# Optimization experiments

Measured on AMD Instinct MI355X. Metric: run time of the kernel, lower is better.

The kernel has to match this reference:

```python
import jax, jax.numpy as jnp
import numpy as np

N_NODES = 100000
N_EDGES = 3200000
D_IN = 256
D_OUT = 256


def setup_inputs() -> dict:
    key = jax.random.key(0)
    k1, k2, k3, k4, k5 = jax.random.split(key, 5)
    x = jax.random.normal(k1, (N_NODES, D_IN), dtype=jnp.float32)
    edge_row = jax.random.randint(k2, (N_EDGES,), 0, N_NODES, dtype=jnp.int32)
    edge_col = jax.random.randint(k3, (N_EDGES,), 0, N_NODES, dtype=jnp.int32)
    # normalized adjacency-like values in (0,1), scaled so rows sum ~1 on average
    edge_val = jax.random.uniform(k4, (N_EDGES,), dtype=jnp.float32) / 32.0
    # kaiming-uniform-like init: bound = sqrt(6 / ((1 + 5) * fan_in)) = 1/sqrt(fan_in)
    bound = 1.0 / np.sqrt(D_IN)
    weight = jax.random.uniform(k5, (D_IN, D_OUT), minval=-bound, maxval=bound, dtype=jnp.float32)
    return {"x": x, "edge_row": edge_row, "edge_col": edge_col,
            "edge_val": edge_val, "weight": weight}


def reference(x, edge_row, edge_col, edge_val, weight):
    # support = P @ X  (sparse COO spmm via gather + segment_sum)
    gathered = edge_val[:, None] * x[edge_col]          # [E, D_IN]
    support = jax.ops.segment_sum(gathered, edge_row, num_segments=N_NODES)  # [N, D_IN]
    # output = relu(support @ W)
    out = jax.nn.relu(support @ weight)                 # [N, D_OUT]
    return out
```

## Files before the change

### kernel.cpp

```cpp
#include <hip/hip_runtime.h>

#define N_NODES 100000
#define N_EDGES 3200000
#define D 256
#define NPAD 100032
#define BCAP 128

#define GEMM_BLKS (NPAD / 64)
#define NCHUNK 782
#define SCAT_BLKS (NCHUNK * 8)
#define ROWS_PER_G 12500

typedef __attribute__((ext_vector_type(8))) short short8;
typedef __attribute__((ext_vector_type(8))) unsigned short ushort8;
typedef __attribute__((ext_vector_type(4))) float f32x4;
typedef __attribute__((ext_vector_type(4))) int i32x4;

static __device__ __forceinline__ unsigned short f2bf(float f) {
  unsigned u = __float_as_uint(f);
  u += 0x7FFF + ((u >> 16) & 1);
  return (unsigned short)(u >> 16);
}
static __device__ __forceinline__ float bf2f(unsigned short h) {
  return __uint_as_float(((unsigned)h) << 16);
}

__global__ __launch_bounds__(64) void convert_wt(
    const float* __restrict__ W, ushort* __restrict__ wt) {
  int n = blockIdx.x;
  int k0 = threadIdx.x * 4;
  ushort4 o;
  o.x = f2bf(W[(size_t)(k0 + 0) * D + n]);
  o.y = f2bf(W[(size_t)(k0 + 1) * D + n]);
  o.z = f2bf(W[(size_t)(k0 + 2) * D + n]);
  o.w = f2bf(W[(size_t)(k0 + 3) * D + n]);
  *(ushort4*)(wt + (size_t)n * D + k0) = o;
}

__global__ __launch_bounds__(256) void gemm_scatter(
    const float* __restrict__ x, const ushort* __restrict__ wt,
    ushort* __restrict__ Y, const int* __restrict__ erow,
    const int* __restrict__ ecol, const float* __restrict__ eval_,
    int* __restrict__ cnt, unsigned* __restrict__ buckets) {
  __shared__ ushort sA[64][264];
  const int tid = threadIdx.x;

  if (blockIdx.x >= GEMM_BLKS) {
    const int sid = blockIdx.x - GEMM_BLKS;
    const int g = blockIdx.x & 7;
    const int chunk = sid >> 3;
    const int lo = g * ROWS_PER_G;
    const int hi = lo + ROWS_PER_G;
    const size_t ebase = (size_t)chunk * 4096;

    #pragma unroll
    for (int q = 0; q < 4; ++q) {
      size_t e0 = ebase + q * 1024 + tid * 4;
      if (e0 >= N_EDGES) continue;
      i32x4 r4 = *(const i32x4*)(erow + e0);
      bool m0 = (r4.x >= lo) & (r4.x < hi);
      bool m1 = (r4.y >= lo) & (r4.y < hi);
      bool m2 = (r4.z >= lo) & (r4.z < hi);
      bool m3 = (r4.w >= lo) & (r4.w < hi);
      if (!(m0 | m1 | m2 | m3)) continue;
      i32x4 c4 = *(const i32x4*)(ecol + e0);
      f32x4 v4 = *(const f32x4*)(eval_ + e0);
      if (m0) {
        int j = atomicAdd(&cnt[r4.x], 1);
        if (j < BCAP)
          buckets[(size_t)r4.x * BCAP + j] =
              ((unsigned)f2bf(v4.x) << 17) | (unsigned)c4.x;
      }
      if (m1) {
        int j = atomicAdd(&cnt[r4.y], 1);
        if (j < BCAP)
          buckets[(size_t)r4.y * BCAP + j] =
              ((unsigned)f2bf(v4.y) << 17) | (unsigned)c4.y;
      }
      if (m2) {
        int j = atomicAdd(&cnt[r4.z], 1);
        if (j < BCAP)
          buckets[(size_t)r4.z * BCAP + j] =
              ((unsigned)f2bf(v4.z) << 17) | (unsigned)c4.z;
      }
      if (m3) {
        int j = atomicAdd(&cnt[r4.w], 1);
        if (j < BCAP)
          buckets[(size_t)r4.w * BCAP + j] =
              ((unsigned)f2bf(v4.w) << 17) | (unsigned)c4.w;
      }
    }
    return;
  }

  const int lane = tid & 63;
  const int wave = tid >> 6;
  const int m0 = blockIdx.x * 64;
  const int lrow = lane & 15;
  const int kch = (lane >> 4) * 8;

  #pragma unroll
  for (int it = 0; it < 16; ++it) {
    int idx = tid + it * 256;
    int row = idx >> 6;
    int c4 = idx & 63;
    int gr = m0 + row;
    if (gr >= N_NODES) gr = N_NODES - 1;
    float4 f = *(const float4*)(x + (size_t)gr * D + c4 * 4);
    ushort4 o;
    o.x = f2bf(f.x); o.y = f2bf(f.y); o.z = f2bf(f.z); o.w = f2bf(f.w);
    *(ushort4*)&sA[row][c4 * 4] = o;
  }
  __syncthreads();

  const int n0 = wave * 64;
  f32x4 acc[4][4];
  #pragma unroll
  for (int i = 0; i < 4; ++i)
    #pragma unroll
    for (int j = 0; j < 4; ++j) acc[i][j] = (f32x4){0.f, 0.f, 0.f, 0.f};

  const ushort* sb = wt + (size_t)(n0 + lrow) * D + kch;

  #pragma unroll
  for (int ks = 0; ks < 8; ++ks) {
    short8 a[4], b[4];
    #pragma unroll
    for (int i = 0; i < 4; ++i) {
      a[i] = *(const short8*)&sA[lrow + i * 16][kch + ks * 32];
      b[i] = *(const short8*)(sb + (size_t)i * 16 * D + ks * 32);
    }
    #pragma unroll
    for (int mi = 0; mi < 4; ++mi)
      #pragma unroll
      for (int ni = 0; ni < 4; ++ni)
        acc[mi][ni] = __builtin_amdgcn_mfma_f32_16x16x32_bf16(
            a[mi], b[ni], acc[mi][ni], 0, 0, 0);
  }

  #pragma unroll
  for (int mi = 0; mi < 4; ++mi) {
    int rbase = m0 + mi * 16 + (lane >> 4) * 4;
    #pragma unroll
    for (int ni = 0; ni < 4; ++ni) {
      int col = n0 + ni * 16 + lrow;
      #pragma unroll
      for (int j = 0; j < 4; ++j)
        Y[(size_t)(rbase + j) * D + col] = f2bf(acc[mi][ni][j]);
    }
  }
}

__global__ __launch_bounds__(256) void row_accum_relu(
    const ushort* __restrict__ Y, const unsigned* __restrict__ buckets,
    const int* __restrict__ cnt, float* __restrict__ out) {
  const int lane = threadIdx.x & 63;
  const int l5 = lane & 31;
  const int sub = lane >> 5;
  int r = (int)((blockIdx.x << 2) + (threadIdx.x >> 6));
  r = __builtin_amdgcn_readfirstlane(r);
  if (r >= N_NODES) return;
  const unsigned* __restrict__ bk = buckets + (size_t)r * BCAP;
  const int end = min(cnt[r], BCAP);
  const int eo = l5 * 8;

  float acc[8] = {0.f, 0.f, 0.f, 0.f, 0.f, 0.f, 0.f, 0.f};

  int p = 0;
  for (; p + 8 <= end; p += 8) {
    uint2 q0 = *(const uint2*)(bk + p);
    uint2 q1 = *(const uint2*)(bk + p + 2);
    uint2 q2 = *(const uint2*)(bk + p + 4);
    uint2 q3 = *(const uint2*)(bk + p + 6);
    unsigned m0 = sub ? q0.y : q0.x;
    unsigned m1 = sub ? q1.y : q1.x;
    unsigned m2 = sub ? q2.y : q2.x;
    unsigned m3 = sub ? q3.y : q3.x;
    ushort8 g0 = *(const ushort8*)(Y + (size_t)(m0 & 0x1FFFF) * D + eo);
    ushort8 g1 = *(const ushort8*)(Y + (size_t)(m1 & 0x1FFFF) * D + eo);
    ushort8 g2 = *(const ushort8*)(Y + (size_t)(m2 & 0x1FFFF) * D + eo);
    ushort8 g3 = *(const ushort8*)(Y + (size_t)(m3 & 0x1FFFF) * D + eo);
    float v0 = __uint_as_float((m0 >> 17) << 16);
    float v1 = __uint_as_float((m1 >> 17) << 16);
    float v2 = __uint_as_float((m2 >> 17) << 16);
    float v3 = __uint_as_float((m3 >> 17) << 16);
    #pragma unroll
    for (int i = 0; i < 8; ++i) acc[i] = fmaf(v0, bf2f(g0[i]), acc[i]);
    #pragma unroll
    for (int i = 0; i < 8; ++i) acc[i] = fmaf(v1, bf2f(g1[i]), acc[i]);
    #pragma unroll
    for (int i = 0; i < 8; ++i) acc[i] = fmaf(v2, bf2f(g2[i]), acc[i]);
    #pragma unroll
    for (int i = 0; i < 8; ++i) acc[i] = fmaf(v3, bf2f(g3[i]), acc[i]);
  }
  for (; p < end; p += 2) {
    uint2 q = *(const uint2*)(bk + p);
    unsigned m = (p + sub < end) ? (sub ? q.y : q.x) : 0u;
    float v = __uint_as_float((m >> 17) << 16);
    ushort8 g = *(const ushort8*)(Y + (size_t)(m & 0x1FFFF) * D + eo);
    #pragma unroll
    for (int i = 0; i < 8; ++i) acc[i] = fmaf(v, bf2f(g[i]), acc[i]);
  }

  #pragma unroll
  for (int i = 0; i < 8; ++i) acc[i] += __shfl_xor(acc[i], 32, 64);

  float4 o;
  if (sub == 0) o = make_float4(acc[0], acc[1], acc[2], acc[3]);
  else          o = make_float4(acc[4], acc[5], acc[6], acc[7]);
  o.x = fmaxf(o.x, 0.f); o.y = fmaxf(o.y, 0.f);
  o.z = fmaxf(o.z, 0.f); o.w = fmaxf(o.w, 0.f);
  *(float4*)(out + (size_t)r * D + eo + sub * 4) = o;
}

__global__ __launch_bounds__(256) void hist_kernel(
    const int* __restrict__ erow, int* __restrict__ cnt) {
  int stride = gridDim.x * blockDim.x;
  for (int e = blockIdx.x * blockDim.x + threadIdx.x; e < N_EDGES; e += stride)
    atomicAdd(&cnt[erow[e]], 1);
}

__global__ __launch_bounds__(1024) void scan_kernel(
    int* __restrict__ cnt, int* __restrict__ row_ptr) {
  __shared__ int partial[1024];
  const int T = 1024;
  const int per = (N_NODES + T - 1) / T;
  int tid = threadIdx.x;
  int base = tid * per;
  int sum = 0;
  for (int i = 0; i < per; ++i) {
    int idx = base + i;
    if (idx < N_NODES) sum += cnt[idx];
  }
  partial[tid] = sum;
  __syncthreads();
  for (int off = 1; off < T; off <<= 1) {
    int v = (tid >= off) ? partial[tid - off] : 0;
    __syncthreads();
    partial[tid] += v;
    __syncthreads();
  }
  int run = (tid == 0) ? 0 : partial[tid - 1];
  for (int i = 0; i < per; ++i) {
    int idx = base + i;
    if (idx < N_NODES) {
      row_ptr[idx] = run;
      run += cnt[idx];
      cnt[idx] = 0;
    }
  }
  if (tid == T - 1) row_ptr[N_NODES] = run;
}

__global__ __launch_bounds__(256) void sort_scatter_kernel(
    const int* __restrict__ erow, const int* __restrict__ ecol,
    const float* __restrict__ eval_, const int* __restrict__ row_ptr,
    int* __restrict__ cursor, int2* __restrict__ sorted) {
  int e = blockIdx.x * blockDim.x + threadIdx.x;
  if (e >= N_EDGES) return;
  int r = erow[e];
  int pos = row_ptr[r] + atomicAdd(&cursor[r], 1);
  sorted[pos] = make_int2(ecol[e], __float_as_int(eval_[e]));
}

__global__ __launch_bounds__(256) void row_accum_kernel(
    const float* __restrict__ x, const int2* __restrict__ sorted,
    const int* __restrict__ row_ptr, float* __restrict__ support) {
  int lane = threadIdx.x & 63;
  int r = (int)((blockIdx.x * blockDim.x + threadIdx.x) >> 6);
  if (r >= N_NODES) return;
  int beg = row_ptr[r];
  int end = row_ptr[r + 1];
  const float4* __restrict__ x4 = (const float4*)x;
  float4 acc = make_float4(0.f, 0.f, 0.f, 0.f);
  int p = beg;
  for (; p + 1 < end; p += 2) {
    int2 cv0 = sorted[p];
    int2 cv1 = sorted[p + 1];
    float4 xv0 = x4[(size_t)cv0.x * 64 + lane];
    float4 xv1 = x4[(size_t)cv1.x * 64 + lane];
    float v0 = __int_as_float(cv0.y);
    float v1 = __int_as_float(cv1.y);
    acc.x = fmaf(v0, xv0.x, acc.x); acc.y = fmaf(v0, xv0.y, acc.y);
    acc.z = fmaf(v0, xv0.z, acc.z); acc.w = fmaf(v0, xv0.w, acc.w);
    acc.x = fmaf(v1, xv1.x, acc.x); acc.y = fmaf(v1, xv1.y, acc.y);
    acc.z = fmaf(v1, xv1.z, acc.z); acc.w = fmaf(v1, xv1.w, acc.w);
  }
  if (p < end) {
    int2 cv = sorted[p];
    float v = __int_as_float(cv.y);
    float4 xv = x4[(size_t)cv.x * 64 + lane];
    acc.x = fmaf(v, xv.x, acc.x); acc.y = fmaf(v, xv.y, acc.y);
    acc.z = fmaf(v, xv.z, acc.z); acc.w = fmaf(v, xv.w, acc.w);
  }
  ((float4*)support)[(size_t)r * 64 + lane] = acc;
}

__global__ __launch_bounds__(256) void scatter_kernel(
    const float* __restrict__ x, const int* __restrict__ erow,
    const int* __restrict__ ecol, const float* __restrict__ eval_,
    float* __restrict__ support, int nwaves) {
  int lane = threadIdx.x & 63;
  int wave = __builtin_amdgcn_readfirstlane(
      (int)((blockIdx.x * blockDim.x + threadIdx.x) >> 6));
  for (int e = wave; e < N_EDGES; e += nwaves) {
    int r = erow[e];
    int c = ecol[e];
    float v = eval_[e];
    float4 xv = ((const float4*)(x + (size_t)c * D))[lane];
    float* dst = support + (size_t)r * D + lane * 4;
    atomicAdd(dst + 0, v * xv.x);
    atomicAdd(dst + 1, v * xv.y);
    atomicAdd(dst + 2, v * xv.z);
    atomicAdd(dst + 3, v * xv.w);
  }
}

__global__ __launch_bounds__(256) void gemm_relu_inplace(
    const float* __restrict__ W, float* __restrict__ io) {
  __shared__ float s[32][D];
  const int tid = threadIdx.x;
  const int row0 = blockIdx.x * 32;
  {
    const float4* src = (const float4*)(io + (size_t)row0 * D);
    float4* sd = (float4*)&s[0][0];
    #pragma unroll
    for (int t = 0; t < 8; ++t) sd[tid + t * 256] = src[tid + t * 256];
  }
  __syncthreads();
  const int j0 = (tid & 63) * 4;
  const int i0 = (tid >> 6) * 8;
  float acc[8][4];
  #pragma unroll
  for (int i = 0; i < 8; ++i)
    for (int q = 0; q < 4; ++q) acc[i][q] = 0.f;
  #pragma unroll 4
  for (int k = 0; k < D; ++k) {
    float4 w4 = *(const float4*)(W + (size_t)k * D + j0);
    #pragma unroll
    for (int i = 0; i < 8; ++i) {
      float sv = s[i0 + i][k];
      acc[i][0] = fmaf(sv, w4.x, acc[i][0]);
      acc[i][1] = fmaf(sv, w4.y, acc[i][1]);
      acc[i][2] = fmaf(sv, w4.z, acc[i][2]);
      acc[i][3] = fmaf(sv, w4.w, acc[i][3]);
    }
  }
  #pragma unroll
  for (int i = 0; i < 8; ++i) {
    float4 o;
    o.x = fmaxf(acc[i][0], 0.f);
    o.y = fmaxf(acc[i][1], 0.f);
    o.z = fmaxf(acc[i][2], 0.f);
    o.w = fmaxf(acc[i][3], 0.f);
    *(float4*)(io + (size_t)(row0 + i0 + i) * D + j0) = o;
  }
}

extern "C" void kernel_launch(void* const* d_in, const int* in_sizes, int n_in,
                              void* d_out, int out_size, void* d_ws, size_t ws_size,
                              hipStream_t stream) {
  const float* x     = (const float*)d_in[0];
  const int*   erow  = (const int*)d_in[1];
  const int*   ecol  = (const int*)d_in[2];
  const float* eval_ = (const float*)d_in[3];
  const float* W     = (const float*)d_in[4];
  float* out = (float*)d_out;

  const size_t cnt_b      = (size_t)N_NODES * sizeof(int);
  const size_t off_bkt    = ((cnt_b + 63) / 64) * 64;
  const size_t bkt_b      = (size_t)N_NODES * BCAP * 4;
  const size_t off_Y      = off_bkt + bkt_b;
  const size_t Y_b        = (size_t)NPAD * D * 2;
  const size_t off_wt     = off_Y + Y_b;
  const size_t wt_b       = (size_t)D * D * 2;
  const size_t need_A     = off_wt + wt_b;

  const size_t rp_b       = (size_t)(N_NODES + 1) * sizeof(int);
  const size_t off_sorted = ((cnt_b + rp_b + 15) / 16) * 16;
  const size_t sortedB_b  = (size_t)(N_EDGES + 2) * 8;
  const size_t need_B     = off_sorted + sortedB_b;

  if (ws_size >= need_A) {
    int*      cnt     = (int*)d_ws;
    unsigned* buckets = (unsigned*)((char*)d_ws + off_bkt);
    ushort*   Y       = (ushort*)((char*)d_ws + off_Y);
    ushort*   wt      = (ushort*)((char*)d_ws + off_wt);

    hipMemsetAsync(cnt, 0, cnt_b, stream);
    convert_wt<<<D, 64, 0, stream>>>(W, wt);
    gemm_scatter<<<GEMM_BLKS + SCAT_BLKS, 256, 0, stream>>>(
        x, wt, Y, erow, ecol, eval_, cnt, buckets);
    row_accum_relu<<<(N_NODES + 3) / 4, 256, 0, stream>>>(
        Y, buckets, cnt, out);
  } else if (ws_size >= need_B) {
    int*  cnt     = (int*)d_ws;
    int*  row_ptr = (int*)((char*)d_ws + cnt_b);
    int2* sorted  = (int2*)((char*)d_ws + off_sorted);

    hipMemsetAsync(cnt, 0, cnt_b, stream);
    hist_kernel<<<2048, 256, 0, stream>>>(erow, cnt);
    scan_kernel<<<1, 1024, 0, stream>>>(cnt, row_ptr);
    sort_scatter_kernel<<<(N_EDGES + 255) / 256, 256, 0, stream>>>(
        erow, ecol, eval_, row_ptr, cnt, sorted);
    row_accum_kernel<<<(N_NODES * 64 + 255) / 256, 256, 0, stream>>>(
        x, sorted, row_ptr, out);
    gemm_relu_inplace<<<N_NODES / 32, 256, 0, stream>>>(W, out);
  } else {
    hipMemsetAsync(out, 0, (size_t)N_NODES * D * sizeof(float), stream);
    const int blocks = 2048;
    const int nwaves = blocks * (256 / 64);
    scatter_kernel<<<blocks, 256, 0, stream>>>(x, erow, ecol, eval_, out, nwaves);
    gemm_relu_inplace<<<N_NODES / 32, 256, 0, stream>>>(W, out);
  }
}
```

Before: 426.1 us.

## Pre-partition edges into row stripes before bucket scatter, fuse weight conversion

Adds a partition pass that bins edges into eight row stripes using shared-memory counters and one global atomic per stripe per block. The scatter stage then reads only its own stripe's compacted list, instead of every one of eight groups re-reading all edge rows and filtering. The weight bf16 conversion is folded into the partition kernel's launch. In exchange there is an extra pass that writes and reads an 8-byte-per-edge staging list. The fixed per-stripe capacity could silently drop edges if a stripe overflows.

Measured after the change: 487.4 us. 14.4% more time.

```diff
diff --git a/kernel.cpp b/kernel.cpp
--- a/kernel.cpp
+++ b/kernel.cpp
@@ -7,9 +7,12 @@
 #define BCAP 128
 
 #define GEMM_BLKS (NPAD / 64)
-#define NCHUNK 782
-#define SCAT_BLKS (NCHUNK * 8)
-#define ROWS_PER_G 12500
+#define PART_BLKS 782
+#define CONV_BLKS 64
+#define SCAT2_BLKS 768
+#define GSTRIDE (96 * 256)
+#define STRIPE 12500
+#define SCAP 412000
 
 typedef __attribute__((ext_vector_type(8))) short short8;
 typedef __attribute__((ext_vector_type(8))) unsigned short ushort8;
@@ -25,70 +28,92 @@
   return __uint_as_float(((unsigned)h) << 16);
 }
 
-__global__ __launch_bounds__(64) void convert_wt(
-    const float* __restrict__ W, ushort* __restrict__ wt) {
-  int n = blockIdx.x;
-  int k0 = threadIdx.x * 4;
-  ushort4 o;
-  o.x = f2bf(W[(size_t)(k0 + 0) * D + n]);
-  o.y = f2bf(W[(size_t)(k0 + 1) * D + n]);
-  o.z = f2bf(W[(size_t)(k0 + 2) * D + n]);
-  o.w = f2bf(W[(size_t)(k0 + 3) * D + n]);
-  *(ushort4*)(wt + (size_t)n * D + k0) = o;
+__global__ __launch_bounds__(256) void part_conv(
+    const int* __restrict__ erow, const int* __restrict__ ecol,
+    const float* __restrict__ eval_, int* __restrict__ scursor,
+    uint2* __restrict__ slist, const float* __restrict__ W,
+    ushort* __restrict__ wt) {
+  const int tid = threadIdx.x;
+  if (blockIdx.x >= PART_BLKS) {
+    int n = (blockIdx.x - PART_BLKS) * 4 + (tid >> 6);
+    int k0 = (tid & 63) * 4;
+    ushort4 o;
+    o.x = f2bf(W[(size_t)(k0 + 0) * D + n]);
+    o.y = f2bf(W[(size_t)(k0 + 1) * D + n]);
+    o.z = f2bf(W[(size_t)(k0 + 2) * D + n]);
+    o.w = f2bf(W[(size_t)(k0 + 3) * D + n]);
+    *(ushort4*)(wt + (size_t)n * D + k0) = o;
+    return;
+  }
+
+  __shared__ int lcnt[8], lbase[8];
+  if (tid < 8) lcnt[tid] = 0;
+  __syncthreads();
+
+  int rank[16];
+  const size_t ebase = (size_t)blockIdx.x * 4096;
+
+  #pragma unroll
+  for (int q = 0; q < 4; ++q) {
+    size_t e0 = ebase + q * 1024 + tid * 4;
+    if (e0 >= N_EDGES) continue;
+    i32x4 r4 = *(const i32x4*)(erow + e0);
+    rank[q * 4 + 0] = atomicAdd(&lcnt[r4.x / STRIPE], 1);
+    rank[q * 4 + 1] = atomicAdd(&lcnt[r4.y / STRIPE], 1);
+    rank[q * 4 + 2] = atomicAdd(&lcnt[r4.z / STRIPE], 1);
+    rank[q * 4 + 3] = atomicAdd(&lcnt[r4.w / STRIPE], 1);
+  }
+  __syncthreads();
+  if (tid < 8) lbase[tid] = atomicAdd(&scursor[tid], lcnt[tid]);
+  __syncthreads();
+
+  #pragma unroll
+  for (int q = 0; q < 4; ++q) {
+    size_t e0 = ebase + q * 1024 + tid * 4;
+    if (e0 >= N_EDGES) continue;
+    i32x4 r4 = *(const i32x4*)(erow + e0);
+    i32x4 c4 = *(const i32x4*)(ecol + e0);
+    f32x4 v4 = *(const f32x4*)(eval_ + e0);
+    int s, p;
+    s = r4.x / STRIPE; p = lbase[s] + rank[q * 4 + 0];
+    if (p < SCAP)
+      slist[(size_t)s * SCAP + p] =
+          make_uint2((unsigned)r4.x, ((unsigned)f2bf(v4.x) << 17) | (unsigned)c4.x);
+    s = r4.y / STRIPE; p = lbase[s] + rank[q * 4 + 1];
+    if (p < SCAP)
+      slist[(size_t)s * SCAP + p] =
+          make_uint2((unsigned)r4.y, ((unsigned)f2bf(v4.y) << 17) | (unsigned)c4.y);
+    s = r4.z / STRIPE; p = lbase[s] + rank[q * 4 + 2];
+    if (p < SCAP)
+      slist[(size_t)s * SCAP + p] =
+          make_uint2((unsigned)r4.z, ((unsigned)f2bf(v4.z) << 17) | (unsigned)c4.z);
+    s = r4.w / STRIPE; p = lbase[s] + rank[q * 4 + 3];
+    if (p < SCAP)
+      slist[(size_t)s * SCAP + p] =
+          make_uint2((unsigned)r4.w, ((unsigned)f2bf(v4.w) << 17) | (unsigned)c4.w);
+  }
 }
 
 __global__ __launch_bounds__(256) void gemm_scatter(
     const float* __restrict__ x, const ushort* __restrict__ wt,
-    ushort* __restrict__ Y, const int* __restrict__ erow,
-    const int* __restrict__ ecol, const float* __restrict__ eval_,
-    int* __restrict__ cnt, unsigned* __restrict__ buckets) {
+    ushort* __restrict__ Y, const int* __restrict__ scursor,
+    const uint2* __restrict__ slist, int* __restrict__ cnt,
+    unsigned* __restrict__ buckets) {
   __shared__ ushort sA[64][264];
   const int tid = threadIdx.x;
 
   if (blockIdx.x >= GEMM_BLKS) {
     const int sid = blockIdx.x - GEMM_BLKS;
-    const int g = blockIdx.x & 7;
-    const int chunk = sid >> 3;
-    const int lo = g * ROWS_PER_G;
-    const int hi = lo + ROWS_PER_G;
-    const size_t ebase = (size_t)chunk * 4096;
-
-    #pragma unroll
-    for (int q = 0; q < 4; ++q) {
-      size_t e0 = ebase + q * 1024 + tid * 4;
-      if (e0 >= N_EDGES) continue;
-      i32x4 r4 = *(const i32x4*)(erow + e0);
-      bool m0 = (r4.x >= lo) & (r4.x < hi);
-      bool m1 = (r4.y >= lo) & (r4.y < hi);
-      bool m2 = (r4.z >= lo) & (r4.z < hi);
-      bool m3 = (r4.w >= lo) & (r4.w < hi);
-      if (!(m0 | m1 | m2 | m3)) continue;
-      i32x4 c4 = *(const i32x4*)(ecol + e0);
-      f32x4 v4 = *(const f32x4*)(eval_ + e0);
-      if (m0) {
-        int j = atomicAdd(&cnt[r4.x], 1);
-        if (j < BCAP)
-          buckets[(size_t)r4.x * BCAP + j] =
-              ((unsigned)f2bf(v4.x) << 17) | (unsigned)c4.x;
-      }
-      if (m1) {
-        int j = atomicAdd(&cnt[r4.y], 1);
-        if (j < BCAP)
-          buckets[(size_t)r4.y * BCAP + j] =
-              ((unsigned)f2bf(v4.y) << 17) | (unsigned)c4.y;
-      }
-      if (m2) {
-        int j = atomicAdd(&cnt[r4.z], 1);
-        if (j < BCAP)
-          buckets[(size_t)r4.z * BCAP + j] =
-              ((unsigned)f2bf(v4.z) << 17) | (unsigned)c4.z;
-      }
-      if (m3) {
-        int j = atomicAdd(&cnt[r4.w], 1);
-        if (j < BCAP)
-          buckets[(size_t)r4.w * BCAP + j] =
-              ((unsigned)f2bf(v4.w) << 17) | (unsigned)c4.w;
-      }
+    const int g = sid & 7;
+    const int sub = sid >> 3;
+    int n = scursor[g];
+    if (n > SCAP) n = SCAP;
+    const uint2* __restrict__ sl = slist + (size_t)g * SCAP;
+    for (int i = sub * 256 + tid; i < n; i += GSTRIDE) {
+      uint2 e = sl[i];
+      int r = (int)e.x;
+      int j = atomicAdd(&cnt[r], 1);
+      if (j < BCAP) buckets[(size_t)r * BCAP + j] = e.y;
     }
     return;
   }
@@ -367,14 +392,17 @@
   const float* W     = (const float*)d_in[4];
   float* out = (float*)d_out;
 
-  const size_t cnt_b      = (size_t)N_NODES * sizeof(int);
-  const size_t off_bkt    = ((cnt_b + 63) / 64) * 64;
-  const size_t bkt_b      = (size_t)N_NODES * BCAP * 4;
-  const size_t off_Y      = off_bkt + bkt_b;
-  const size_t Y_b        = (size_t)NPAD * D * 2;
-  const size_t off_wt     = off_Y + Y_b;
-  const size_t wt_b       = (size_t)D * D * 2;
-  const size_t need_A     = off_wt + wt_b;
+  const size_t cnt_b    = (size_t)N_NODES * sizeof(int);
+  const size_t off_scur = cnt_b;
+  const size_t off_sl   = off_scur + 64;
+  const size_t sl_b     = (size_t)8 * SCAP * 8;
+  const size_t off_bkt  = ((off_sl + sl_b + 63) / 64) * 64;
+  const size_t bkt_b    = (size_t)N_NODES * BCAP * 4;
+  const size_t off_Y    = off_bkt + bkt_b;
+  const size_t Y_b      = (size_t)NPAD * D * 2;
+  const size_t off_wt   = off_Y + Y_b;
+  const size_t wt_b     = (size_t)D * D * 2;
+  const size_t need_A   = off_wt + wt_b;
 
   const size_t rp_b       = (size_t)(N_NODES + 1) * sizeof(int);
   const size_t off_sorted = ((cnt_b + rp_b + 15) / 16) * 16;
@@ -383,14 +411,17 @@
 
   if (ws_size >= need_A) {
     int*      cnt     = (int*)d_ws;
+    int*      scursor = (int*)((char*)d_ws + off_scur);
+    uint2*    slist   = (uint2*)((char*)d_ws + off_sl);
     unsigned* buckets = (unsigned*)((char*)d_ws + off_bkt);
     ushort*   Y       = (ushort*)((char*)d_ws + off_Y);
     ushort*   wt      = (ushort*)((char*)d_ws + off_wt);
 
-    hipMemsetAsync(cnt, 0, cnt_b, stream);
-    convert_wt<<<D, 64, 0, stream>>>(W, wt);
-    gemm_scatter<<<GEMM_BLKS + SCAT_BLKS, 256, 0, stream>>>(
-        x, wt, Y, erow, ecol, eval_, cnt, buckets);
+    hipMemsetAsync(d_ws, 0, cnt_b + 64, stream);
+    part_conv<<<PART_BLKS + CONV_BLKS, 256, 0, stream>>>(
+        erow, ecol, eval_, scursor, slist, W, wt);
+    gemm_scatter<<<GEMM_BLKS + SCAT2_BLKS, 256, 0, stream>>>(
+        x, wt, Y, scursor, slist, cnt, buckets);
     row_accum_relu<<<(N_NODES + 3) / 4, 256, 0, stream>>>(
         Y, buckets, cnt, out);
   } else if (ws_size >= need_B) {
```
